# Kernel tuning notes

Hardware: AMD Instinct MI355X
Metric: run time of the kernel (lower is better)

The kernel has to match this reference:

```python
import jax, jax.numpy as jnp
import numpy as np
from jax import lax

B, T, I, H, N = 8192, 100, 24, 64, 8  # batch, seq_len, input_size, hidden_size, hidden_neurons
H2 = 2 * H


def setup_inputs() -> dict:
    key = jax.random.key(0)
    ks = iter(jax.random.split(key, 80))
    d = {"input_seq": jax.random.normal(next(ks), (B, T, I), jnp.float32)}
    def triple(name, shape):
        d[name + "_mu"] = 0.1 * jax.random.normal(next(ks), shape, jnp.float32)
        d[name + "_rho"] = -6.0 + 0.1 * jax.random.normal(next(ks), shape, jnp.float32)
        d[name + "_eps"] = jax.random.normal(next(ks), shape, jnp.float32)
    # BayesianLSTM params: weight_ih (in, 4H), weight_hh (H, 4H), bias (4H,)
    triple("l1_wih", (I, 4 * H)); triple("l1_whh", (H, 4 * H)); triple("l1_b", (4 * H,))
    triple("l2_wih", (H, 4 * H2)); triple("l2_whh", (H2, 4 * H2)); triple("l2_b", (4 * H2,))
    # BayesianLinear params: weight (out, in), bias (out,)
    triple("fc1_w", (N, H2)); triple("fc1_b", (N,))
    triple("fc2_w", (N, N)); triple("fc2_b", (N,))
    triple("out_w", (1, N)); triple("out_b", (1,))
    return d


def _sample(mu, rho, eps):
    # blitz reparameterization: sigma = log1p(exp(rho))
    return mu + jnp.log1p(jnp.exp(rho)) * eps


def _lstm(x, wih, whh, b):
    # x: [B, T, in]; returns full hidden sequence [B, T, Hn]; gate order i,f,g,o
    Hn = whh.shape[0]
    xg = jnp.einsum('bti,ig->btg', x, wih) + b  # precompute input projection
    def step(carry, xg_t):
        h, c = carry
        gates = xg_t + h @ whh
        i, f, g, o = jnp.split(gates, 4, axis=-1)
        c = jax.nn.sigmoid(f) * c + jax.nn.sigmoid(i) * jnp.tanh(g)
        h = jax.nn.sigmoid(o) * jnp.tanh(c)
        return (h, c), h
    h0 = jnp.zeros((x.shape[0], Hn), x.dtype)
    _, hs = lax.scan(step, (h0, h0), jnp.swapaxes(xg, 0, 1))
    return jnp.swapaxes(hs, 0, 1)


def _forward(input_seq,
             l1_wih_mu, l1_wih_rho, l1_wih_eps, l1_whh_mu, l1_whh_rho, l1_whh_eps,
             l1_b_mu, l1_b_rho, l1_b_eps,
             l2_wih_mu, l2_wih_rho, l2_wih_eps, l2_whh_mu, l2_whh_rho, l2_whh_eps,
             l2_b_mu, l2_b_rho, l2_b_eps,
             fc1_w_mu, fc1_w_rho, fc1_w_eps, fc1_b_mu, fc1_b_rho, fc1_b_eps,
             fc2_w_mu, fc2_w_rho, fc2_w_eps, fc2_b_mu, fc2_b_rho, fc2_b_eps,
             out_w_mu, out_w_rho, out_w_eps, out_b_mu, out_b_rho, out_b_eps):
    w1i = _sample(l1_wih_mu, l1_wih_rho, l1_wih_eps)
    w1h = _sample(l1_whh_mu, l1_whh_rho, l1_whh_eps)
    b1 = _sample(l1_b_mu, l1_b_rho, l1_b_eps)
    w2i = _sample(l2_wih_mu, l2_wih_rho, l2_wih_eps)
    w2h = _sample(l2_whh_mu, l2_whh_rho, l2_whh_eps)
    b2 = _sample(l2_b_mu, l2_b_rho, l2_b_eps)
    fc1w = _sample(fc1_w_mu, fc1_w_rho, fc1_w_eps); fc1b = _sample(fc1_b_mu, fc1_b_rho, fc1_b_eps)
    fc2w = _sample(fc2_w_mu, fc2_w_rho, fc2_w_eps); fc2b = _sample(fc2_b_mu, fc2_b_rho, fc2_b_eps)
    outw = _sample(out_w_mu, out_w_rho, out_w_eps); outb = _sample(out_b_mu, out_b_rho, out_b_eps)

    h1 = _lstm(input_seq, w1i, w1h, b1)      # [B, T, H]
    h2 = _lstm(h1, w2i, w2h, b2)             # [B, T, 2H]
    out = h2[:, -1, :]                       # [B, 2H]
    x = jax.nn.relu(out @ fc1w.T + fc1b)
    x = jax.nn.relu(x @ fc2w.T + fc2b)
    y = x @ outw.T + outb                    # [B, 1]
    return y.reshape(-1)


def reference(input_seq,
              l1_wih_mu, l1_wih_rho, l1_wih_eps, l1_whh_mu, l1_whh_rho, l1_whh_eps,
              l1_b_mu, l1_b_rho, l1_b_eps,
              l2_wih_mu, l2_wih_rho, l2_wih_eps, l2_whh_mu, l2_whh_rho, l2_whh_eps,
              l2_b_mu, l2_b_rho, l2_b_eps,
              fc1_w_mu, fc1_w_rho, fc1_w_eps, fc1_b_mu, fc1_b_rho, fc1_b_eps,
              fc2_w_mu, fc2_w_rho, fc2_w_eps, fc2_b_mu, fc2_b_rho, fc2_b_eps,
              out_w_mu, out_w_rho, out_w_eps, out_b_mu, out_b_rho, out_b_eps):
    return _forward(input_seq,
                    l1_wih_mu, l1_wih_rho, l1_wih_eps, l1_whh_mu, l1_whh_rho, l1_whh_eps,
                    l1_b_mu, l1_b_rho, l1_b_eps,
                    l2_wih_mu, l2_wih_rho, l2_wih_eps, l2_whh_mu, l2_whh_rho, l2_whh_eps,
                    l2_b_mu, l2_b_rho, l2_b_eps,
                    fc1_w_mu, fc1_w_rho, fc1_w_eps, fc1_b_mu, fc1_b_rho, fc1_b_eps,
                    fc2_w_mu, fc2_w_rho, fc2_w_eps, fc2_b_mu, fc2_b_rho, fc2_b_eps,
                    out_w_mu, out_w_rho, out_w_eps, out_b_mu, out_b_rho, out_b_eps)
```

## Files before the change

### kernel.cpp

```cpp
#include <hip/hip_runtime.h>
#include <math.h>


typedef __attribute__((ext_vector_type(8))) short short8;
typedef __attribute__((ext_vector_type(4))) float f32x4;

#define MFMA16(a, b, c) __builtin_amdgcn_mfma_f32_16x16x32_bf16((a), (b), (c), 0, 0, 0)

#define WS_W1G_OFF 196608
#define WS_WF_OFF  245760

struct SampParams {
  const float* w1i[3]; const float* w1h[3]; const float* b1[3];
  const float* w2i[3]; const float* w2h[3]; const float* b2[3];
  const float* f1w[3]; const float* f1b[3];
  const float* f2w[3]; const float* f2b[3];
  const float* ow[3];  const float* ob[3];
  short* W2S; short* W1G; float* WF;
};

struct LstmParams {
  const float* input;
  const short* W2S; const short* W1G; const float* WF;
  float* out;
};

__device__ __forceinline__ float softplus_fast(float x) {
  float e = __builtin_amdgcn_exp2f(1.44269504f * x);
  return 0.69314718f * __builtin_amdgcn_logf(1.0f + e);
}

__device__ __forceinline__ float samp(const float* const q[3], int idx) {
  return q[0][idx] + softplus_fast(q[1][idx]) * q[2][idx];
}

__device__ __forceinline__ short f2bf(float f) {
  unsigned u = __float_as_uint(f);
  unsigned r = (u + 0x7FFFu + ((u >> 16) & 1u)) >> 16;
  return (short)r;
}

__device__ __forceinline__ unsigned cvt_pk_bf16(float lo, float hi) {
  unsigned r;
  asm("v_cvt_pk_bf16_f32 %0, %1, %2" : "=v"(r) : "v"(lo), "v"(hi));
  return r;
}

__device__ __forceinline__ void lstm_elem(float gi, float gf, float gg, float go,
                                          float& c, float& h) {
  float A = 1.0f + __builtin_amdgcn_exp2f(-1.44269504f * gi);
  float B = 1.0f + __builtin_amdgcn_exp2f(-1.44269504f * gf);
  float r = __builtin_amdgcn_rcpf(A * B);
  float si = r * B;
  float sf = r * A;
  float C = 1.0f + __builtin_amdgcn_exp2f(2.88539008f * gg);
  float D = 1.0f + __builtin_amdgcn_exp2f(-1.44269504f * go);
  float r2 = __builtin_amdgcn_rcpf(C * D);
  float tg = 1.0f - 2.0f * (r2 * D);
  float so = r2 * C;
  float cn = sf * c + si * tg;
  c = cn;
  float E = 1.0f + __builtin_amdgcn_exp2f(2.88539008f * cn);
  h = so * (1.0f - 2.0f * __builtin_amdgcn_rcpf(E));
}

__global__ __launch_bounds__(256) void sample_kernel(SampParams p)
{
  int i = blockIdx.x * 256 + threadIdx.x;
  if (i < 12288) {
    int tid = i & 511, gg = (i >> 9) & 3, kk = i >> 11;
    int quad = (tid >> 4) & 3, col = tid & 15, v0 = (tid >> 6) * 16;
    int c = gg * 128 + v0 + col;
    short8 v;
#pragma unroll
    for (int j = 0; j < 8; ++j) {
      int k = kk * 32 + quad * 8 + j;
      float x = (k < 64) ? samp(p.w2i, k * 512 + c) : samp(p.w2h, (k - 64) * 512 + c);
      v[j] = f2bf(x);
    }
    *(short8*)&p.W2S[i * 8] = v;
  } else if (i < 15360) {
    int u = i - 12288;
    int slice = u >> 8, n = u & 255;
    int k0 = (slice >> 2) * 32 + (slice & 3) * 8;
    short8 v;
#pragma unroll
    for (int j = 0; j < 8; ++j) {
      int k = k0 + j;
      float x = 0.0f;
      if (k < 24)       x = samp(p.w1i, k * 256 + n);
      else if (k >= 32) x = samp(p.w1h, (k - 32) * 256 + n);
      v[j] = f2bf(x);
    }
    *(short8*)&p.W1G[u * 8] = v;
  } else if (i < 17241) {
    int u = i - 15360;
    float x;
    if (u < 256)       x = samp(p.b1,  u);
    else if (u < 768)  x = samp(p.b2,  u - 256);
    else if (u < 1792) x = samp(p.f1w, u - 768);
    else if (u < 1856) x = samp(p.f2w, u - 1792);
    else if (u < 1864) x = samp(p.f1b, u - 1856);
    else if (u < 1872) x = samp(p.f2b, u - 1864);
    else if (u < 1880) x = samp(p.ow,  u - 1872);
    else               x = samp(p.ob,  0);
    p.WF[u] = x;
  }
}


__global__ __launch_bounds__(512, 2)
void blstm_kernel(LstmParams p)
{
  __shared__ __align__(16) unsigned char pool[79872];
  short* const W1L = (short*)pool;
  short* const A1b = (short*)(pool + 49152);
  short* const A2b = (short*)(pool + 62464);

  const int tid  = threadIdx.x;
  const int w    = tid >> 6;
  const int l    = tid & 63;
  const int quad = l >> 4;
  const int col  = l & 15;
  const int b0   = blockIdx.x * 32;

  const int wq = w & 3;
  const int mh = w >> 2;
  const int v0 = w * 16;

  const short8* const W2v = (const short8*)p.W2S;
  short8 w2r[24];
#pragma unroll
  for (int f = 0; f < 24; ++f) w2r[f] = W2v[f * 512 + tid];

#pragma unroll
  for (int r = 0; r < 6; ++r) {
    short8 v = *(const short8*)&p.W1G[(r * 512 + tid) * 8];
    *(short8*)&W1L[(r * 512 + tid) * 8] = v;
  }

  float b1v[4], b2v[4];
#pragma unroll
  for (int g = 0; g < 4; ++g) b1v[g] = p.WF[g * 64 + wq * 16 + col];
#pragma unroll
  for (int g = 0; g < 4; ++g) b2v[g] = p.WF[256 + g * 128 + v0 + col];

  for (int i = tid; i < 6656; i += 512) A1b[i] = 0;
  for (int i = tid; i < 8704; i += 512) A2b[i] = 0;
  __syncthreads();

  int xr = 0, xi = 0;
  const bool xln = tid < 384;
  const float* xptr = p.input;
  if (xln) {
    int e = tid * 2; xr = e / 24; xi = e - xr * 24;
    const float* base = p.input + (size_t)(b0 + xr) * 2400 + xi;
    float2 xv = *(const float2*)base;
    *(unsigned*)&A1b[xr * 104 + xi] = cvt_pk_bf16(xv.x, xv.y);
    xptr = base + 24;
  }
  __syncthreads();

  float c1a[4]  = {0.f, 0.f, 0.f, 0.f};
  float c2a[2][4] = {{0.f,0.f,0.f,0.f},{0.f,0.f,0.f,0.f}};
  float hf2[2][4];

  const int a1rd = (mh * 16 + col) * 104;

  auto step = [&](const short* __restrict__ A1r, const short* __restrict__ A2r,
                  short* __restrict__ A1w, short* __restrict__ A2w, bool dox) {
    const bool do_x = dox && xln;
    float2 xv;
    if (do_x) xv = *(const float2*)xptr;

    short8 aA0 = *(const short8*)&A1r[a1rd +      quad * 8];
    short8 aA1 = *(const short8*)&A1r[a1rd + 32 + quad * 8];
    short8 aA2 = *(const short8*)&A1r[a1rd + 64 + quad * 8];
    f32x4 g1[4];
#pragma unroll
    for (int g = 0; g < 4; ++g) {
      f32x4 acc = (f32x4){b1v[g], b1v[g], b1v[g], b1v[g]};
      acc = MFMA16(aA0, *(const short8*)&W1L[(((0 * 4 + quad) << 8) + g * 64 + wq * 16 + col) * 8], acc);
      acc = MFMA16(aA1, *(const short8*)&W1L[(((1 * 4 + quad) << 8) + g * 64 + wq * 16 + col) * 8], acc);
      acc = MFMA16(aA2, *(const short8*)&W1L[(((2 * 4 + quad) << 8) + g * 64 + wq * 16 + col) * 8], acc);
      g1[g] = acc;
    }

    {
      float h1v[4];
#pragma unroll
      for (int i = 0; i < 4; ++i)
        lstm_elem(g1[0][i], g1[1][i], g1[2][i], g1[3][i], c1a[i], h1v[i]);
      int base = (mh * 16 + quad * 4) * 104 + 32 + wq * 16 + col;
      unsigned pkA = cvt_pk_bf16(h1v[0], h1v[1]);
      unsigned pkB = cvt_pk_bf16(h1v[2], h1v[3]);
      A1w[base]       = (short)pkA;
      A1w[base + 104] = (short)(pkA >> 16);
      A1w[base + 208] = (short)pkB;
      A1w[base + 312] = (short)(pkB >> 16);
    }
    if (do_x)
      *(unsigned*)&A1w[xr * 104 + xi] = cvt_pk_bf16(xv.x, xv.y);

    f32x4 g2[2][4];
#pragma unroll
    for (int g = 0; g < 4; ++g) {
      g2[0][g] = (f32x4){b2v[g], b2v[g], b2v[g], b2v[g]};
      g2[1][g] = g2[0][g];
    }
#pragma unroll
    for (int kk = 0; kk < 6; ++kk) {
      short8 a0, a1f;
      if (kk < 2) {
        a0  = *(const short8*)&A1r[      col  * 104 + 32 + kk * 32 + quad * 8];
        a1f = *(const short8*)&A1r[(16 + col) * 104 + 32 + kk * 32 + quad * 8];
      } else {
        int o = (kk - 2) * 32 + quad * 8;
        a0  = *(const short8*)&A2r[      col  * 136 + o];
        a1f = *(const short8*)&A2r[(16 + col) * 136 + o];
      }
#pragma unroll
      for (int g = 0; g < 4; ++g) {
        g2[0][g] = MFMA16(a0,  w2r[kk * 4 + g], g2[0][g]);
        g2[1][g] = MFMA16(a1f, w2r[kk * 4 + g], g2[1][g]);
      }
    }

    {
      int u2 = v0 + col;
#pragma unroll
      for (int mi = 0; mi < 2; ++mi) {
        float hv[4];
#pragma unroll
        for (int i = 0; i < 4; ++i) {
          lstm_elem(g2[mi][0][i], g2[mi][1][i], g2[mi][2][i], g2[mi][3][i],
                    c2a[mi][i], hv[i]);
          hf2[mi][i] = hv[i];
        }
        unsigned pkA = cvt_pk_bf16(hv[0], hv[1]);
        unsigned pkB = cvt_pk_bf16(hv[2], hv[3]);
        int base = (mi * 16 + quad * 4) * 136 + u2;
        A2w[base]       = (short)pkA;
        A2w[base + 136] = (short)(pkA >> 16);
        A2w[base + 272] = (short)pkB;
        A2w[base + 408] = (short)(pkB >> 16);
      }
    }
  };

  short* const A1_0 = A1b;            short* const A1_1 = A1b + 3328;
  short* const A2_0 = A2b;            short* const A2_1 = A2b + 4352;

  {
    float2 xv;
    if (xln) xv = *(const float2*)xptr;
    short8 aA0 = *(const short8*)&A1_0[a1rd +      quad * 8];
    short8 aA1 = *(const short8*)&A1_0[a1rd + 32 + quad * 8];
    short8 aA2 = *(const short8*)&A1_0[a1rd + 64 + quad * 8];
    f32x4 g1[4];
#pragma unroll
    for (int g = 0; g < 4; ++g) {
      f32x4 acc = (f32x4){b1v[g], b1v[g], b1v[g], b1v[g]};
      acc = MFMA16(aA0, *(const short8*)&W1L[(((0 * 4 + quad) << 8) + g * 64 + wq * 16 + col) * 8], acc);
      acc = MFMA16(aA1, *(const short8*)&W1L[(((1 * 4 + quad) << 8) + g * 64 + wq * 16 + col) * 8], acc);
      acc = MFMA16(aA2, *(const short8*)&W1L[(((2 * 4 + quad) << 8) + g * 64 + wq * 16 + col) * 8], acc);
      g1[g] = acc;
    }
    float h1v[4];
#pragma unroll
    for (int i = 0; i < 4; ++i)
      lstm_elem(g1[0][i], g1[1][i], g1[2][i], g1[3][i], c1a[i], h1v[i]);
    int base = (mh * 16 + quad * 4) * 104 + 32 + wq * 16 + col;
    unsigned pkA = cvt_pk_bf16(h1v[0], h1v[1]);
    unsigned pkB = cvt_pk_bf16(h1v[2], h1v[3]);
    A1_1[base]       = (short)pkA;
    A1_1[base + 104] = (short)(pkA >> 16);
    A1_1[base + 208] = (short)pkB;
    A1_1[base + 312] = (short)(pkB >> 16);
    if (xln)
      *(unsigned*)&A1_1[xr * 104 + xi] = cvt_pk_bf16(xv.x, xv.y);
    __syncthreads();
    xptr += 24;
  }

  for (int jj = 1; jj <= 99; jj += 2) {
    step(A1_1, A2_1, A1_0, A2_0, jj <= 98);
    __syncthreads();
    xptr += 24;
    step(A1_0, A2_0, A1_1, A2_1, jj + 1 <= 98);
    __syncthreads();
    xptr += 24;
  }

  float* const H2   = (float*)pool;
  float* const FC1W = (float*)(pool + 16896);
  float* const FC2W = (float*)(pool + 20992);
  float* const FB1  = (float*)(pool + 21248);
  float* const FB2  = (float*)(pool + 21280);
  float* const OWp  = (float*)(pool + 21312);
  float* const OBp  = (float*)(pool + 21344);
  float* const X1   = (float*)(pool + 21376);
  float* const X2   = (float*)(pool + 22400);

  {
    int u2 = v0 + col;
#pragma unroll
    for (int mi = 0; mi < 2; ++mi)
#pragma unroll
      for (int i = 0; i < 4; ++i) {
        int row = mi * 16 + quad * 4 + i;
        H2[row * 132 + u2] = hf2[mi][i];
      }
  }
  for (int i = tid; i < 1024; i += 512) FC1W[i] = p.WF[768 + i];
  if (tid < 64)               FC2W[tid]     = p.WF[1792 + tid];
  if (tid >= 64 && tid < 72)  FB1[tid - 64] = p.WF[1856 + tid - 64];
  if (tid >= 72 && tid < 80)  FB2[tid - 72] = p.WF[1864 + tid - 72];
  if (tid >= 80 && tid < 88)  OWp[tid - 80] = p.WF[1872 + tid - 80];
  if (tid == 88)              OBp[0]        = p.WF[1880];
  __syncthreads();

  if (tid < 256) {
    int row = tid >> 3, o = tid & 7;
    float s = FB1[o];
#pragma unroll 8
    for (int k = 0; k < 128; ++k) s += H2[row * 132 + k] * FC1W[o * 128 + k];
    X1[tid] = fmaxf(s, 0.0f);
  }
  __syncthreads();
  if (tid < 256) {
    int row = tid >> 3, o = tid & 7;
    float s = FB2[o];
#pragma unroll
    for (int k = 0; k < 8; ++k) s += X1[row * 8 + k] * FC2W[o * 8 + k];
    X2[tid] = fmaxf(s, 0.0f);
  }
  __syncthreads();
  if (tid < 32) {
    float s = OBp[0];
#pragma unroll
    for (int k = 0; k < 8; ++k) s += X2[tid * 8 + k] * OWp[k];
    p.out[b0 + tid] = s;
  }
}

extern "C" void kernel_launch(void* const* d_in, const int* in_sizes, int n_in,
                              void* d_out, int out_size, void* d_ws, size_t ws_size,
                              hipStream_t stream)
{
  (void)in_sizes; (void)n_in; (void)ws_size; (void)out_size;

  SampParams sp;
  const float** grp[12] = { sp.w1i, sp.w1h, sp.b1, sp.w2i, sp.w2h, sp.b2,
                            sp.f1w, sp.f1b, sp.f2w, sp.f2b, sp.ow, sp.ob };
  int idx = 1;
  for (int t = 0; t < 12; ++t)
    for (int j = 0; j < 3; ++j)
      grp[t][j] = (const float*)d_in[idx++];
  sp.W2S = (short*)d_ws;
  sp.W1G = (short*)((char*)d_ws + WS_W1G_OFF);
  sp.WF  = (float*)((char*)d_ws + WS_WF_OFF);

  LstmParams bp;
  bp.input = (const float*)d_in[0];
  bp.W2S = (const short*)d_ws;
  bp.W1G = (const short*)((char*)d_ws + WS_W1G_OFF);
  bp.WF  = (const float*)((char*)d_ws + WS_WF_OFF);
  bp.out = (float*)d_out;

  sample_kernel<<<dim3(68), dim3(256), 0, stream>>>(sp);
  blstm_kernel<<<dim3(256), dim3(512), 0, stream>>>(bp);
}
```

Baseline: 400.0 us.

## Pair-vectorize LSTM cell math, prefetch input one step ahead, split sampling threads

The LSTM cell is rewritten to work on pairs of elements as float2 vectors so the compiler can emit packed FP32 ops. The c update is merged into one rational expression with a single reciprocal, the h reciprocals of two lanes share one rcp, and exp arguments are clamped to keep the merged products from overflowing. The input x for the next step is now loaded one step ahead to hide global-load latency, and the sampling kernel gives each thread half as many W2 elements, with more blocks launched. Fusing the reciprocals changes rounding slightly and adds clamp ops.

After: 416.5 us. +4.1%, slower.

```diff
diff --git a/kernel.cpp b/kernel.cpp
--- a/kernel.cpp
+++ b/kernel.cpp
@@ -4,6 +4,7 @@
 
 typedef __attribute__((ext_vector_type(8))) short short8;
 typedef __attribute__((ext_vector_type(4))) float f32x4;
+typedef __attribute__((ext_vector_type(2))) float f32x2;
 
 #define MFMA16(a, b, c) __builtin_amdgcn_mfma_f32_16x16x32_bf16((a), (b), (c), 0, 0, 0)
 
@@ -46,41 +47,68 @@
   return r;
 }
 
-__device__ __forceinline__ void lstm_elem(float gi, float gf, float gg, float go,
-                                          float& c, float& h) {
-  float A = 1.0f + __builtin_amdgcn_exp2f(-1.44269504f * gi);
-  float B = 1.0f + __builtin_amdgcn_exp2f(-1.44269504f * gf);
-  float r = __builtin_amdgcn_rcpf(A * B);
-  float si = r * B;
-  float sf = r * A;
-  float C = 1.0f + __builtin_amdgcn_exp2f(2.88539008f * gg);
-  float D = 1.0f + __builtin_amdgcn_exp2f(-1.44269504f * go);
-  float r2 = __builtin_amdgcn_rcpf(C * D);
-  float tg = 1.0f - 2.0f * (r2 * D);
-  float so = r2 * C;
-  float cn = sf * c + si * tg;
-  c = cn;
-  float E = 1.0f + __builtin_amdgcn_exp2f(2.88539008f * cn);
-  h = so * (1.0f - 2.0f * __builtin_amdgcn_rcpf(E));
+__device__ __forceinline__ f32x2 exp2v(f32x2 x) {
+  f32x2 r;
+  r.x = __builtin_amdgcn_exp2f(x.x);
+  r.y = __builtin_amdgcn_exp2f(x.y);
+  return r;
+}
+
+__device__ __forceinline__ f32x2 clampv(f32x2 x, float lim) {
+  f32x2 lo = {-lim, -lim}, hi = {lim, lim};
+  return __builtin_elementwise_min(__builtin_elementwise_max(x, lo), hi);
+}
+
+__device__ __forceinline__ void lstm_pair(f32x2 gi, f32x2 gf, f32x2 gg, f32x2 go,
+                                          f32x2& c, f32x2& h) {
+  const f32x2 kneg = {-1.44269504f, -1.44269504f};
+  const f32x2 kpos = { 2.88539008f,  2.88539008f};
+  const f32x2 one  = {1.0f, 1.0f};
+  f32x2 a  = exp2v(clampv(gi * kneg, 20.2f));
+  f32x2 b  = exp2v(clampv(gf * kneg, 20.2f));
+  f32x2 cv = exp2v(clampv(gg * kpos, 40.4f));
+  f32x2 d  = exp2v(clampv(go * kneg, 20.2f));
+  f32x2 A = one + a, B = one + b, Cv = one + cv, D = one + d;
+  f32x2 AC  = A * Cv;
+  f32x2 Ncn = (cv - one) * B + c * AC;
+  f32x2 Dcn = AC * B;
+  f32x2 rq;
+  rq.x = __builtin_amdgcn_rcpf(Dcn.x);
+  rq.y = __builtin_amdgcn_rcpf(Dcn.y);
+  c = Ncn * rq;
+  f32x2 e  = exp2v(clampv(c * kpos, 40.4f));
+  f32x2 Dh = D + D * e;
+  f32x2 Nh = e - one;
+  float R = __builtin_amdgcn_rcpf(Dh.x * Dh.y);
+  h.x = Nh.x * (R * Dh.y);
+  h.y = Nh.y * (R * Dh.x);
 }
 
 __global__ __launch_bounds__(256) void sample_kernel(SampParams p)
 {
   int i = blockIdx.x * 256 + threadIdx.x;
-  if (i < 12288) {
-    int tid = i & 511, gg = (i >> 9) & 3, kk = i >> 11;
+  if (i < 24576) {
+    int f = i >> 1, half = i & 1;
+    int tid = f & 511, gg = (f >> 9) & 3, kk = f >> 11;
     int quad = (tid >> 4) & 3, col = tid & 15, v0 = (tid >> 6) * 16;
     int c = gg * 128 + v0 + col;
-    short8 v;
-#pragma unroll
-    for (int j = 0; j < 8; ++j) {
-      int k = kk * 32 + quad * 8 + j;
-      float x = (k < 64) ? samp(p.w2i, k * 512 + c) : samp(p.w2h, (k - 64) * 512 + c);
-      v[j] = f2bf(x);
-    }
-    *(short8*)&p.W2S[i * 8] = v;
-  } else if (i < 15360) {
-    int u = i - 12288;
+    int j0 = half * 4;
+    unsigned o0, o1;
+    {
+      int k = kk * 32 + quad * 8 + j0;
+      float x0 = (k < 64) ? samp(p.w2i, k * 512 + c) : samp(p.w2h, (k - 64) * 512 + c);
+      ++k;
+      float x1 = (k < 64) ? samp(p.w2i, k * 512 + c) : samp(p.w2h, (k - 64) * 512 + c);
+      ++k;
+      float x2 = (k < 64) ? samp(p.w2i, k * 512 + c) : samp(p.w2h, (k - 64) * 512 + c);
+      ++k;
+      float x3 = (k < 64) ? samp(p.w2i, k * 512 + c) : samp(p.w2h, (k - 64) * 512 + c);
+      o0 = cvt_pk_bf16(x0, x1);
+      o1 = cvt_pk_bf16(x2, x3);
+    }
+    *(uint2*)&p.W2S[f * 8 + j0] = make_uint2(o0, o1);
+  } else if (i < 27648) {
+    int u = i - 24576;
     int slice = u >> 8, n = u & 255;
     int k0 = (slice >> 2) * 32 + (slice & 3) * 8;
     short8 v;
@@ -93,8 +121,8 @@
       v[j] = f2bf(x);
     }
     *(short8*)&p.W1G[u * 8] = v;
-  } else if (i < 17241) {
-    int u = i - 15360;
+  } else if (i < 29529) {
+    int u = i - 27648;
     float x;
     if (u < 256)       x = samp(p.b1,  u);
     else if (u < 768)  x = samp(p.b2,  u - 256);
@@ -155,23 +183,24 @@
   if (xln) {
     int e = tid * 2; xr = e / 24; xi = e - xr * 24;
     const float* base = p.input + (size_t)(b0 + xr) * 2400 + xi;
-    float2 xv = *(const float2*)base;
-    *(unsigned*)&A1b[xr * 104 + xi] = cvt_pk_bf16(xv.x, xv.y);
+    float2 xv0 = *(const float2*)base;
+    *(unsigned*)&A1b[xr * 104 + xi] = cvt_pk_bf16(xv0.x, xv0.y);
     xptr = base + 24;
   }
   __syncthreads();
 
-  float c1a[4]  = {0.f, 0.f, 0.f, 0.f};
-  float c2a[2][4] = {{0.f,0.f,0.f,0.f},{0.f,0.f,0.f,0.f}};
-  float hf2[2][4];
+  f32x2 c1p[2] = {{0.f, 0.f}, {0.f, 0.f}};
+  f32x2 c2p[2][2] = {{{0.f,0.f},{0.f,0.f}}, {{0.f,0.f},{0.f,0.f}}};
+  f32x2 hf2p[2][2];
+
+  float2 xv_w, xv_n;
 
   const int a1rd = (mh * 16 + col) * 104;
 
   auto step = [&](const short* __restrict__ A1r, const short* __restrict__ A2r,
-                  short* __restrict__ A1w, short* __restrict__ A2w, bool dox) {
-    const bool do_x = dox && xln;
-    float2 xv;
-    if (do_x) xv = *(const float2*)xptr;
+                  short* __restrict__ A1w, short* __restrict__ A2w,
+                  bool w_x, bool l_x) {
+    if (l_x && xln) xv_n = *(const float2*)xptr;
 
     short8 aA0 = *(const short8*)&A1r[a1rd +      quad * 8];
     short8 aA1 = *(const short8*)&A1r[a1rd + 32 + quad * 8];
@@ -187,20 +216,23 @@
     }
 
     {
-      float h1v[4];
-#pragma unroll
-      for (int i = 0; i < 4; ++i)
-        lstm_elem(g1[0][i], g1[1][i], g1[2][i], g1[3][i], c1a[i], h1v[i]);
+      f32x2 h01, h23;
+      lstm_pair((f32x2){g1[0][0], g1[0][1]}, (f32x2){g1[1][0], g1[1][1]},
+                (f32x2){g1[2][0], g1[2][1]}, (f32x2){g1[3][0], g1[3][1]},
+                c1p[0], h01);
+      lstm_pair((f32x2){g1[0][2], g1[0][3]}, (f32x2){g1[1][2], g1[1][3]},
+                (f32x2){g1[2][2], g1[2][3]}, (f32x2){g1[3][2], g1[3][3]},
+                c1p[1], h23);
       int base = (mh * 16 + quad * 4) * 104 + 32 + wq * 16 + col;
-      unsigned pkA = cvt_pk_bf16(h1v[0], h1v[1]);
-      unsigned pkB = cvt_pk_bf16(h1v[2], h1v[3]);
+      unsigned pkA = cvt_pk_bf16(h01.x, h01.y);
+      unsigned pkB = cvt_pk_bf16(h23.x, h23.y);
       A1w[base]       = (short)pkA;
       A1w[base + 104] = (short)(pkA >> 16);
       A1w[base + 208] = (short)pkB;
       A1w[base + 312] = (short)(pkB >> 16);
     }
-    if (do_x)
-      *(unsigned*)&A1w[xr * 104 + xi] = cvt_pk_bf16(xv.x, xv.y);
+    if (w_x && xln)
+      *(unsigned*)&A1w[xr * 104 + xi] = cvt_pk_bf16(xv_w.x, xv_w.y);
 
     f32x4 g2[2][4];
 #pragma unroll
@@ -230,15 +262,17 @@
       int u2 = v0 + col;
 #pragma unroll
       for (int mi = 0; mi < 2; ++mi) {
-        float hv[4];
-#pragma unroll
-        for (int i = 0; i < 4; ++i) {
-          lstm_elem(g2[mi][0][i], g2[mi][1][i], g2[mi][2][i], g2[mi][3][i],
-                    c2a[mi][i], hv[i]);
-          hf2[mi][i] = hv[i];
-        }
-        unsigned pkA = cvt_pk_bf16(hv[0], hv[1]);
-        unsigned pkB = cvt_pk_bf16(hv[2], hv[3]);
+        f32x2 h01, h23;
+        lstm_pair((f32x2){g2[mi][0][0], g2[mi][0][1]}, (f32x2){g2[mi][1][0], g2[mi][1][1]},
+                  (f32x2){g2[mi][2][0], g2[mi][2][1]}, (f32x2){g2[mi][3][0], g2[mi][3][1]},
+                  c2p[mi][0], h01);
+        lstm_pair((f32x2){g2[mi][0][2], g2[mi][0][3]}, (f32x2){g2[mi][1][2], g2[mi][1][3]},
+                  (f32x2){g2[mi][2][2], g2[mi][2][3]}, (f32x2){g2[mi][3][2], g2[mi][3][3]},
+                  c2p[mi][1], h23);
+        hf2p[mi][0] = h01;
+        hf2p[mi][1] = h23;
+        unsigned pkA = cvt_pk_bf16(h01.x, h01.y);
+        unsigned pkB = cvt_pk_bf16(h23.x, h23.y);
         int base = (mi * 16 + quad * 4) * 136 + u2;
         A2w[base]       = (short)pkA;
         A2w[base + 136] = (short)(pkA >> 16);
@@ -246,14 +280,17 @@
         A2w[base + 408] = (short)(pkB >> 16);
       }
     }
+    xv_w = xv_n;
   };
 
   short* const A1_0 = A1b;            short* const A1_1 = A1b + 3328;
   short* const A2_0 = A2b;            short* const A2_1 = A2b + 4352;
 
   {
-    float2 xv;
-    if (xln) xv = *(const float2*)xptr;
+    if (xln) {
+      xv_w = *(const float2*)xptr;
+      xv_n = *(const float2*)(xptr + 24);
+    }
     short8 aA0 = *(const short8*)&A1_0[a1rd +      quad * 8];
     short8 aA1 = *(const short8*)&A1_0[a1rd + 32 + quad * 8];
     short8 aA2 = *(const short8*)&A1_0[a1rd + 64 + quad * 8];
@@ -266,28 +303,32 @@
       acc = MFMA16(aA2, *(const short8*)&W1L[(((2 * 4 + quad) << 8) + g * 64 + wq * 16 + col) * 8], acc);
       g1[g] = acc;
     }
-    float h1v[4];
-#pragma unroll
-    for (int i = 0; i < 4; ++i)
-      lstm_elem(g1[0][i], g1[1][i], g1[2][i], g1[3][i], c1a[i], h1v[i]);
+    f32x2 h01, h23;
+    lstm_pair((f32x2){g1[0][0], g1[0][1]}, (f32x2){g1[1][0], g1[1][1]},
+              (f32x2){g1[2][0], g1[2][1]}, (f32x2){g1[3][0], g1[3][1]},
+              c1p[0], h01);
+    lstm_pair((f32x2){g1[0][2], g1[0][3]}, (f32x2){g1[1][2], g1[1][3]},
+              (f32x2){g1[2][2], g1[2][3]}, (f32x2){g1[3][2], g1[3][3]},
+              c1p[1], h23);
     int base = (mh * 16 + quad * 4) * 104 + 32 + wq * 16 + col;
-    unsigned pkA = cvt_pk_bf16(h1v[0], h1v[1]);
-    unsigned pkB = cvt_pk_bf16(h1v[2], h1v[3]);
+    unsigned pkA = cvt_pk_bf16(h01.x, h01.y);
+    unsigned pkB = cvt_pk_bf16(h23.x, h23.y);
     A1_1[base]       = (short)pkA;
     A1_1[base + 104] = (short)(pkA >> 16);
     A1_1[base + 208] = (short)pkB;
     A1_1[base + 312] = (short)(pkB >> 16);
     if (xln)
-      *(unsigned*)&A1_1[xr * 104 + xi] = cvt_pk_bf16(xv.x, xv.y);
+      *(unsigned*)&A1_1[xr * 104 + xi] = cvt_pk_bf16(xv_w.x, xv_w.y);
+    __syncthreads();
+    xv_w = xv_n;
+    xptr += 48;
+  }
+
+  for (int jj = 1; jj <= 99; jj += 2) {
+    step(A1_1, A2_1, A1_0, A2_0, jj <= 98, jj <= 97);
     __syncthreads();
     xptr += 24;
-  }
-
-  for (int jj = 1; jj <= 99; jj += 2) {
-    step(A1_1, A2_1, A1_0, A2_0, jj <= 98);
-    __syncthreads();
-    xptr += 24;
-    step(A1_0, A2_0, A1_1, A2_1, jj + 1 <= 98);
+    step(A1_0, A2_0, A1_1, A2_1, jj + 1 <= 98, jj + 1 <= 97);
     __syncthreads();
     xptr += 24;
   }
@@ -305,12 +346,13 @@
   {
     int u2 = v0 + col;
 #pragma unroll
-    for (int mi = 0; mi < 2; ++mi)
-#pragma unroll
-      for (int i = 0; i < 4; ++i) {
-        int row = mi * 16 + quad * 4 + i;
-        H2[row * 132 + u2] = hf2[mi][i];
-      }
+    for (int mi = 0; mi < 2; ++mi) {
+      int row = mi * 16 + quad * 4;
+      H2[(row + 0) * 132 + u2] = hf2p[mi][0].x;
+      H2[(row + 1) * 132 + u2] = hf2p[mi][0].y;
+      H2[(row + 2) * 132 + u2] = hf2p[mi][1].x;
+      H2[(row + 3) * 132 + u2] = hf2p[mi][1].y;
+    }
   }
   for (int i = tid; i < 1024; i += 512) FC1W[i] = p.WF[768 + i];
   if (tid < 64)               FC2W[tid]     = p.WF[1792 + tid];
@@ -368,6 +410,6 @@
   bp.WF  = (const float*)((char*)d_ws + WS_WF_OFF);
   bp.out = (float*)d_out;
 
-  sample_kernel<<<dim3(68), dim3(256), 0, stream>>>(sp);
+  sample_kernel<<<dim3(116), dim3(256), 0, stream>>>(sp);
   blstm_kernel<<<dim3(256), dim3(512), 0, stream>>>(bp);
 }
```
